# Kernel optimization log

Measured on AMD Instinct MI355X. Metric: run time of the kernel, lower is better.

The kernel has to match this reference:

```python
import jax, jax.numpy as jnp
import numpy as np

DIM = 512
HEADS = 8


def setup_inputs() -> dict:
    key = jax.random.key(0)
    k1, k2, k3, k4 = jax.random.split(key, 4)
    head_dim = DIM // HEADS
    scale = head_dim ** -0.5
    x = jax.random.normal(k1, (4, 4096, DIM), dtype=jnp.float32)
    Wqkv = jax.random.normal(k2, (3 * DIM, DIM), dtype=jnp.float32) * (DIM ** -0.5)
    temperature = jnp.ones((HEADS, 1, 1), dtype=jnp.float32) * scale
    Wproj = jax.random.normal(k3, (DIM, DIM), dtype=jnp.float32) * (DIM ** -0.5)
    bproj = jnp.zeros((DIM,), dtype=jnp.float32)
    return {"x": x, "Wqkv": Wqkv, "temperature": temperature, "Wproj": Wproj, "bproj": bproj}


def reference(x, Wqkv, temperature, Wproj, bproj):
    B, N, C = x.shape
    H = temperature.shape[0]
    D = C // H
    qkv = (x @ Wqkv.T).reshape(B, N, 3, H, D).transpose(2, 0, 3, 1, 4)  # (3,B,H,N,D)
    q, k, v = qkv[0], qkv[1], qkv[2]
    q = jax.nn.relu(q)
    k = jax.nn.relu(k)
    # denom = clamp(q @ sum_n k, min=100) -> (B,H,N,1)
    ksum = k.sum(axis=2)  # (B,H,D)
    denom = jnp.clip(jnp.einsum('bhnd,bhd->bhn', q, ksum), 100.0)[..., None]
    # attn = (k^T v) * temperature -> (B,H,D,D)
    attn = jnp.einsum('bhnd,bhne->bhde', k, v) * temperature
    attn1 = jnp.einsum('bhnd,bhde->bhne', q, attn)  # (B,H,N,D)
    out = attn1 / denom
    y = out.transpose(0, 2, 1, 3).reshape(B, N, C) @ Wproj.T + bproj
    return (y, attn1)
```

## Files before the change

### kernel.cpp

```cpp
#include <hip/hip_runtime.h>
#include <cstdint>
#include <cstddef>

typedef _Float16 f16;
typedef _Float16 f16x4 __attribute__((ext_vector_type(4)));
typedef _Float16 f16x8 __attribute__((ext_vector_type(8)));
typedef float f32x4 __attribute__((ext_vector_type(4)));
typedef __fp16 h2 __attribute__((ext_vector_type(2)));

#define MFMA16(a, b, c) __builtin_amdgcn_mfma_f32_16x16x32_f16(a, b, c, 0, 0, 0)

static __device__ __forceinline__ void gld16(const void* g, void* l) {
  __builtin_amdgcn_global_load_lds(
      (const __attribute__((address_space(1))) void*)g,
      (__attribute__((address_space(3))) void*)l, 16, 0, 0);
}

static __device__ __forceinline__ h2 as_h2(uint32_t u) {
  union { uint32_t u; h2 h; } c; c.u = u; return c.h;
}

#define B_ 4
#define N_ 4096
#define C_ 512
#define H_ 8
#define D_ 64
#define BN_ROWS 16384
#define QKV_COLS 1536

__global__ __launch_bounds__(256) void k_convert(
    const float* __restrict__ x, const float* __restrict__ wqkv,
    const float* __restrict__ wproj,
    f16* __restrict__ xh, f16* __restrict__ wqkvh, f16* __restrict__ wprojh)
{
  const int NX  = (BN_ROWS * C_) / 4;
  const int NW1 = (QKV_COLS * C_) / 4;
  const int NW2 = (C_ * C_) / 4;
  const int total = NX + NW1 + NW2;
  const int stride = gridDim.x * blockDim.x;
  for (int i = blockIdx.x * blockDim.x + threadIdx.x; i < total; i += stride) {
    const float4* s; f16x4* d; int j;
    if (i < NX)              { s = (const float4*)x;     d = (f16x4*)xh;     j = i; }
    else if (i < NX + NW1)   { s = (const float4*)wqkv;  d = (f16x4*)wqkvh;  j = i - NX; }
    else                     { s = (const float4*)wproj; d = (f16x4*)wprojh; j = i - NX - NW1; }
    float4 v = s[j];
    f16x4 o; o[0] = (f16)v.x; o[1] = (f16)v.y; o[2] = (f16)v.z; o[3] = (f16)v.w;
    d[j] = o;
  }
}

__global__ __launch_bounds__(256) void k_qkv_gemm(
    const f16* __restrict__ X, const f16* __restrict__ W, f16* __restrict__ Out)
{
  __shared__ f16 As[128][64];
  __shared__ f16 Bs[128][64];
  int w = (blockIdx.x & 7) * 192 + (blockIdx.x >> 3);
  const int n0 = (w % 12) * 128;
  const int m0 = (w / 12) * 128;
  const int tid = threadIdx.x;
  const int wid = tid >> 6;
  const int lane = tid & 63;
  const int lr = lane & 15, lg = lane >> 4;
  const int sr = lane >> 3;
  const int sslot = (lane & 7) ^ sr;
  const int wr = (wid >> 1) * 64, wc = (wid & 1) * 64;
  f32x4 acc[4][4] = {};
  for (int kt = 0; kt < 512; kt += 64) {
#pragma unroll
    for (int i = 0; i < 4; ++i) {
      int chunk = wid * 4 + i;
      int row = chunk * 8 + sr;
      gld16(&X[(size_t)(m0 + row) * 512 + kt + sslot * 8], &As[chunk * 8][0]);
      gld16(&W[(size_t)(n0 + row) * 512 + kt + sslot * 8], &Bs[chunk * 8][0]);
    }
    __syncthreads();
#pragma unroll
    for (int kk = 0; kk < 2; ++kk) {
      f16x8 af[4], bf[4];
#pragma unroll
      for (int m = 0; m < 4; ++m)
        af[m] = *(const f16x8*)&As[wr + m * 16 + lr][(((kk * 4 + lg) ^ (lr & 7)) * 8)];
#pragma unroll
      for (int n = 0; n < 4; ++n)
        bf[n] = *(const f16x8*)&Bs[wc + n * 16 + lr][(((kk * 4 + lg) ^ (lr & 7)) * 8)];
#pragma unroll
      for (int m = 0; m < 4; ++m)
#pragma unroll
        for (int n = 0; n < 4; ++n)
          acc[m][n] = MFMA16(bf[n], af[m], acc[m][n]);
    }
    __syncthreads();
  }
#pragma unroll
  for (int m = 0; m < 4; ++m)
#pragma unroll
    for (int n = 0; n < 4; ++n) {
      int row = m0 + wr + m * 16 + lr;
      int col = n0 + wc + n * 16 + lg * 4;
      f16x4 o;
      bool relu = (col < 1024);
#pragma unroll
      for (int j = 0; j < 4; ++j) {
        float v = acc[m][n][j];
        if (relu) v = fmaxf(v, 0.f);
        o[j] = (f16)v;
      }
      *(f16x4*)&Out[(size_t)row * QKV_COLS + col] = o;
    }
}

__global__ __launch_bounds__(256) void k_ktv(
    const f16* __restrict__ qkv, float* __restrict__ partial, float* __restrict__ pksum)
{
  __shared__ f16 ks[32][64];
  __shared__ f16 vs[32][64];
  const int bh = blockIdx.x, sp = blockIdx.y;
  const int b = bh >> 3, h = bh & 7;
  const int tid = threadIdx.x, wid = tid >> 6, lane = tid & 63;
  const int srow = lane >> 3, scol = (lane & 7) * 8;
  const int td = (wid << 2) | (lane >> 4);
  const int te = lane & 15;
  const uint32_t SEL_LO = 0x05040100u, SEL_HI = 0x07060302u;
  const h2 ones = {(__fp16)1.0f, (__fp16)1.0f};
  float acc[4][4] = {};
  float ksacc[4] = {0.f, 0.f, 0.f, 0.f};
  const size_t rowbase = (size_t)b * N_ + sp * 256;
  for (int t = 0; t < 8; ++t) {
    int nb = t * 32 + wid * 8 + srow;
    gld16(&qkv[(rowbase + nb) * QKV_COLS + 512 + h * 64 + scol], &ks[wid * 8][0]);
    gld16(&qkv[(rowbase + nb) * QKV_COLS + 1024 + h * 64 + scol], &vs[wid * 8][0]);
    __syncthreads();
#pragma unroll 4
    for (int n = 0; n < 32; n += 2) {
      uint2 ka = *(const uint2*)&ks[n][td * 4];
      uint2 kb = *(const uint2*)&ks[n + 1][td * 4];
      uint2 va = *(const uint2*)&vs[n][te * 4];
      uint2 vb = *(const uint2*)&vs[n + 1][te * 4];
      uint32_t kp[4], vp[4];
      kp[0] = __builtin_amdgcn_perm(kb.x, ka.x, SEL_LO);
      kp[1] = __builtin_amdgcn_perm(kb.x, ka.x, SEL_HI);
      kp[2] = __builtin_amdgcn_perm(kb.y, ka.y, SEL_LO);
      kp[3] = __builtin_amdgcn_perm(kb.y, ka.y, SEL_HI);
      vp[0] = __builtin_amdgcn_perm(vb.x, va.x, SEL_LO);
      vp[1] = __builtin_amdgcn_perm(vb.x, va.x, SEL_HI);
      vp[2] = __builtin_amdgcn_perm(vb.y, va.y, SEL_LO);
      vp[3] = __builtin_amdgcn_perm(vb.y, va.y, SEL_HI);
#pragma unroll
      for (int i = 0; i < 4; ++i)
#pragma unroll
        for (int j = 0; j < 4; ++j)
          acc[i][j] = __builtin_amdgcn_fdot2(as_h2(kp[i]), as_h2(vp[j]), acc[i][j], false);
      if (te == 0) {
#pragma unroll
        for (int i = 0; i < 4; ++i)
          ksacc[i] = __builtin_amdgcn_fdot2(as_h2(kp[i]), ones, ksacc[i], false);
      }
    }
    __syncthreads();
  }
  float* pp = partial + (size_t)(bh * 16 + sp) * 4096;
#pragma unroll
  for (int i = 0; i < 4; ++i)
#pragma unroll
    for (int j = 0; j < 4; ++j)
      pp[(td * 4 + i) * 64 + te * 4 + j] = acc[i][j];
  if (te == 0) {
    float* kp2 = pksum + (bh * 16 + sp) * 64;
#pragma unroll
    for (int i = 0; i < 4; ++i) kp2[td * 4 + i] = ksacc[i];
  }
}

__global__ __launch_bounds__(256) void k_reduce(
    const float* __restrict__ partial, const float* __restrict__ pksum,
    float* __restrict__ attn_acc, float* __restrict__ ksum)
{
  const int bh = blockIdx.x, seg = blockIdx.y, tid = threadIdx.x;
  const int i = seg * 256 + tid;
  float s = 0.f;
#pragma unroll 8
  for (int sp = 0; sp < 16; ++sp) s += partial[(size_t)(bh * 16 + sp) * 4096 + i];
  attn_acc[bh * 4096 + i] = s;
  if (seg == 0 && tid < 64) {
    float t2 = 0.f;
#pragma unroll 8
    for (int sp = 0; sp < 16; ++sp) t2 += pksum[(bh * 16 + sp) * 64 + tid];
    ksum[bh * 64 + tid] = t2;
  }
}

__global__ __launch_bounds__(512, 1) void k_attn_proj(
    const f16* __restrict__ qkv, const float* __restrict__ attn_acc,
    const float* __restrict__ ksum, const float* __restrict__ temp,
    const f16* __restrict__ Wp, const float* __restrict__ bias,
    float* __restrict__ attn1_out, float* __restrict__ Y)
{
  __shared__ f16 outs[8][64][64];
  __shared__ union {
    f16 attnT[8][64][64];
    f16 Bs[512][64];
  } u;
  __shared__ float ksum_s[512];
  __shared__ float bias_s[512];
  __shared__ float denom_s[8][64];

  const int bid = blockIdx.x;
  const int b = bid >> 6, sp = bid & 63;
  const size_t gr = (size_t)b * N_ + sp * 64;
  const int tid = threadIdx.x;
  const int wid = tid >> 6, lane = tid & 63;
  const int lr = lane & 15, lg = lane >> 4;
  const int sr = lane >> 3, sslot = (lane & 7) ^ sr;

  ksum_s[tid] = ksum[b * 512 + tid];
  bias_s[tid] = bias[tid];
  __syncthreads();

#define STAGEPB(kc_)                                                          \
  do {                                                                        \
    _Pragma("unroll")                                                         \
    for (int rd = 0; rd < 8; ++rd)                                            \
      gld16(&Wp[(size_t)(wid * 64 + rd * 8 + sr) * 512 + (kc_) * 64 + sslot * 8], \
            &u.Bs[wid * 64 + rd * 8][0]);                                     \
  } while (0)

  {
    const int h = wid;
    const float tsc = temp[h];
#pragma unroll
    for (int rr = 0; rr < 8; ++rr)
      gld16(&qkv[(gr + rr * 8 + sr) * QKV_COLS + h * 64 + sslot * 8],
            &outs[h][rr * 8][0]);
#pragma unroll
    for (int dc = 0; dc < 4; ++dc) {
      float vals[16];
#pragma unroll
      for (int x = 0; x < 16; ++x)
        vals[x] = attn_acc[(size_t)(b * 8 + h) * 4096 + (dc * 16 + x) * 64 + lane] * tsc;
#pragma unroll
      for (int half = 0; half < 2; ++half) {
        int slot = (dc * 2 + half) ^ (lane & 7);
        f16x8 pk;
#pragma unroll
        for (int j = 0; j < 8; ++j) pk[j] = (f16)vals[half * 8 + j];
        *(f16x8*)&u.attnT[h][lane][slot * 8] = pk;
      }
    }
    asm volatile("s_waitcnt vmcnt(0)" ::: "memory");
    {
      const int r = lane;
      float dot = 0.f;
#pragma unroll
      for (int c = 0; c < 8; ++c) {
        f16x8 qv = *(const f16x8*)&outs[h][r][((c ^ (r & 7)) * 8)];
#pragma unroll
        for (int j = 0; j < 8; ++j) dot += (float)qv[j] * ksum_s[h * 64 + c * 8 + j];
      }
      denom_s[h][r] = fmaxf(dot, 100.f);
    }
    f16x8 af[2][4], bf[4][2];
#pragma unroll
    for (int kk = 0; kk < 2; ++kk)
#pragma unroll
      for (int m = 0; m < 4; ++m)
        af[kk][m] = *(const f16x8*)&outs[h][m * 16 + lr][(((kk * 4 + lg) ^ (lr & 7)) * 8)];
#pragma unroll
    for (int et = 0; et < 4; ++et)
#pragma unroll
      for (int kk = 0; kk < 2; ++kk)
        bf[et][kk] = *(const f16x8*)&u.attnT[h][et * 16 + lr][(((kk * 4 + lg) ^ (lr & 7)) * 8)];
    asm volatile("s_waitcnt lgkmcnt(0)" ::: "memory");
    __builtin_amdgcn_sched_barrier(0);
    STAGEPB(0);
    f32x4 acc1[4][4] = {};
    __builtin_amdgcn_s_setprio(1);
#pragma unroll
    for (int kk = 0; kk < 2; ++kk)
#pragma unroll
      for (int m = 0; m < 4; ++m)
#pragma unroll
        for (int et = 0; et < 4; ++et)
          acc1[m][et] = MFMA16(bf[et][kk], af[kk][m], acc1[m][et]);
    __builtin_amdgcn_s_setprio(0);
#pragma unroll
    for (int m = 0; m < 4; ++m) {
      const int rl = m * 16 + lr;
      const float dn = denom_s[h][rl];
#pragma unroll
      for (int et = 0; et < 4; ++et) {
        int e = et * 16 + lg * 4;
        float4 o;
        o.x = acc1[m][et][0]; o.y = acc1[m][et][1]; o.z = acc1[m][et][2]; o.w = acc1[m][et][3];
        *(float4*)&attn1_out[((size_t)(b * 8 + h) * N_ + sp * 64 + rl) * 64 + e] = o;
        f16x4 oh;
#pragma unroll
        for (int j = 0; j < 4; ++j) oh[j] = (f16)(acc1[m][et][j] / dn);
        *(f16x4*)((char*)&outs[h][rl][0] + (((e >> 3) ^ (rl & 7)) * 16) + (lg & 1) * 8) = oh;
      }
    }
  }
  asm volatile("s_waitcnt lgkmcnt(0)" ::: "memory");
  __builtin_amdgcn_s_barrier();
  asm volatile("" ::: "memory");

  f32x4 accP[4][4] = {};
#pragma unroll
  for (int kc = 0; kc < 8; ++kc) {
    asm volatile("s_waitcnt vmcnt(0)" ::: "memory");
    f16x8 bfp[2][4], afp[2][4];
#pragma unroll
    for (int kk = 0; kk < 2; ++kk) {
#pragma unroll
      for (int n = 0; n < 4; ++n)
        bfp[kk][n] = *(const f16x8*)&u.Bs[wid * 64 + n * 16 + lr][(((kk * 4 + lg) ^ (lr & 7)) * 8)];
#pragma unroll
      for (int m = 0; m < 4; ++m)
        afp[kk][m] = *(const f16x8*)&outs[kc][m * 16 + lr][(((kk * 4 + lg) ^ (lr & 7)) * 8)];
    }
    asm volatile("s_waitcnt lgkmcnt(0)" ::: "memory");
    __builtin_amdgcn_sched_barrier(0);
    if (kc < 7) STAGEPB(kc + 1);
    __builtin_amdgcn_s_setprio(1);
#pragma unroll
    for (int kk = 0; kk < 2; ++kk)
#pragma unroll
      for (int m = 0; m < 4; ++m)
#pragma unroll
        for (int n = 0; n < 4; ++n)
          accP[m][n] = MFMA16(bfp[kk][n], afp[kk][m], accP[m][n]);
    __builtin_amdgcn_s_setprio(0);
  }
#undef STAGEPB

#pragma unroll
  for (int m = 0; m < 4; ++m)
#pragma unroll
    for (int n = 0; n < 4; ++n) {
      size_t row = gr + m * 16 + lr;
      int col = wid * 64 + n * 16 + lg * 4;
      float4 o;
      o.x = accP[m][n][0] + bias_s[col + 0];
      o.y = accP[m][n][1] + bias_s[col + 1];
      o.z = accP[m][n][2] + bias_s[col + 2];
      o.w = accP[m][n][3] + bias_s[col + 3];
      *(float4*)&Y[row * C_ + col] = o;
    }
}

extern "C" void kernel_launch(void* const* d_in, const int* in_sizes, int n_in,
                              void* d_out, int out_size, void* d_ws, size_t ws_size,
                              hipStream_t stream)
{
  const float* x     = (const float*)d_in[0];
  const float* wqkv  = (const float*)d_in[1];
  const float* temp  = (const float*)d_in[2];
  const float* wproj = (const float*)d_in[3];
  const float* bproj = (const float*)d_in[4];
  float* y_out     = (float*)d_out;
  float* attn1_out = (float*)d_out + 8388608;

  char* ws = (char*)d_ws;
  f16*   xh       = (f16*)(ws);
  float* partial  = (float*)(ws);
  f16*   wqkvh    = (f16*)(ws + 16777216);
  f16*   wprojh   = (f16*)(ws + 18350080);
  f16*   qkvh     = (f16*)(ws + 18874368);
  float* attn_acc = (float*)(ws + 69206016);
  float* ksum     = (float*)(ws + 69730304);
  float* pksum    = (float*)(ws + 69738496);

  hipLaunchKernelGGL(k_convert,   dim3(2048),   dim3(256), 0, stream, x, wqkv, wproj, xh, wqkvh, wprojh);
  hipLaunchKernelGGL(k_qkv_gemm,  dim3(1536),   dim3(256), 0, stream, xh, wqkvh, qkvh);
  hipLaunchKernelGGL(k_ktv,       dim3(32, 16), dim3(256), 0, stream, qkvh, partial, pksum);
  hipLaunchKernelGGL(k_reduce,    dim3(32, 16), dim3(256), 0, stream, partial, pksum, attn_acc, ksum);
  hipLaunchKernelGGL(k_attn_proj, dim3(256),    dim3(512), 0, stream,
                     qkvh, attn_acc, ksum, temp, wprojh, bproj, attn1_out, y_out);
}
```

Measured before the change: 103.7 us.

## Stream QKV GEMM weight operand directly into registers with double buffering

The QKV GEMM no longer stages the weight tile in LDS. Each wave loads its B fragments straight from global memory into a pair of register buffers, prefetching the next K step while the current one runs MFMAs. Only the X tile goes through LDS, with explicit waitcnt/barrier sync, MFMA priority raising and a 3-blocks-per-SM launch bound. This halves LDS use and LDS read traffic but adds uncoalesced global loads, duplicate reads of W across waves, and more register pressure.

After: 127.0 us. 22.5% more time.

```diff
diff --git a/kernel.cpp b/kernel.cpp
--- a/kernel.cpp
+++ b/kernel.cpp
@@ -49,11 +49,10 @@
   }
 }
 
-__global__ __launch_bounds__(256) void k_qkv_gemm(
+__global__ __launch_bounds__(256, 3) void k_qkv_gemm(
     const f16* __restrict__ X, const f16* __restrict__ W, f16* __restrict__ Out)
 {
   __shared__ f16 As[128][64];
-  __shared__ f16 Bs[128][64];
   int w = (blockIdx.x & 7) * 192 + (blockIdx.x >> 3);
   const int n0 = (w % 12) * 128;
   const int m0 = (w / 12) * 128;
@@ -64,33 +63,64 @@
   const int sr = lane >> 3;
   const int sslot = (lane & 7) ^ sr;
   const int wr = (wid >> 1) * 64, wc = (wid & 1) * 64;
+  const f16* bbase0 = &W[(size_t)(n0 + wc + 0 * 16 + lr) * 512 + lg * 8];
+  const f16* bbase1 = &W[(size_t)(n0 + wc + 1 * 16 + lr) * 512 + lg * 8];
+  const f16* bbase2 = &W[(size_t)(n0 + wc + 2 * 16 + lr) * 512 + lg * 8];
+  const f16* bbase3 = &W[(size_t)(n0 + wc + 3 * 16 + lr) * 512 + lg * 8];
   f32x4 acc[4][4] = {};
-  for (int kt = 0; kt < 512; kt += 64) {
+  f16x8 bfE[2][4], bfO[2][4];
+
+#define LOADB(dst, tt)                                                        \
+  do {                                                                        \
+    _Pragma("unroll")                                                         \
+    for (int kk = 0; kk < 2; ++kk) {                                          \
+      dst[kk][0] = *(const f16x8*)(bbase0 + (tt) * 64 + kk * 32);             \
+      dst[kk][1] = *(const f16x8*)(bbase1 + (tt) * 64 + kk * 32);             \
+      dst[kk][2] = *(const f16x8*)(bbase2 + (tt) * 64 + kk * 32);             \
+      dst[kk][3] = *(const f16x8*)(bbase3 + (tt) * 64 + kk * 32);             \
+    }                                                                         \
+  } while (0)
+
+  LOADB(bfE, 0);
+
+#pragma unroll
+  for (int t = 0; t < 8; ++t) {
 #pragma unroll
     for (int i = 0; i < 4; ++i) {
       int chunk = wid * 4 + i;
       int row = chunk * 8 + sr;
-      gld16(&X[(size_t)(m0 + row) * 512 + kt + sslot * 8], &As[chunk * 8][0]);
-      gld16(&W[(size_t)(n0 + row) * 512 + kt + sslot * 8], &Bs[chunk * 8][0]);
-    }
-    __syncthreads();
+      gld16(&X[(size_t)(m0 + row) * 512 + t * 64 + sslot * 8], &As[chunk * 8][0]);
+    }
+    asm volatile("s_waitcnt vmcnt(0)" ::: "memory");
+    __builtin_amdgcn_s_barrier();
+    asm volatile("" ::: "memory");
+    if (t < 7) {
+      if ((t & 1) == 0) LOADB(bfO, t + 1);
+      else              LOADB(bfE, t + 1);
+    }
 #pragma unroll
     for (int kk = 0; kk < 2; ++kk) {
-      f16x8 af[4], bf[4];
+      f16x8 af[4];
 #pragma unroll
       for (int m = 0; m < 4; ++m)
         af[m] = *(const f16x8*)&As[wr + m * 16 + lr][(((kk * 4 + lg) ^ (lr & 7)) * 8)];
-#pragma unroll
-      for (int n = 0; n < 4; ++n)
-        bf[n] = *(const f16x8*)&Bs[wc + n * 16 + lr][(((kk * 4 + lg) ^ (lr & 7)) * 8)];
+      __builtin_amdgcn_s_setprio(1);
 #pragma unroll
       for (int m = 0; m < 4; ++m)
 #pragma unroll
         for (int n = 0; n < 4; ++n)
-          acc[m][n] = MFMA16(bf[n], af[m], acc[m][n]);
-    }
-    __syncthreads();
-  }
+          acc[m][n] = ((t & 1) == 0) ? MFMA16(bfE[kk][n], af[m], acc[m][n])
+                                     : MFMA16(bfO[kk][n], af[m], acc[m][n]);
+      __builtin_amdgcn_s_setprio(0);
+    }
+    if (t < 7) {
+      asm volatile("s_waitcnt lgkmcnt(0)" ::: "memory");
+      __builtin_amdgcn_s_barrier();
+      asm volatile("" ::: "memory");
+    }
+  }
+#undef LOADB
+
 #pragma unroll
   for (int m = 0; m < 4; ++m)
 #pragma unroll
```
